# Performance work log

Hardware: AMD Instinct MI355X
Metric: run time of the kernel (lower is better)

The kernel has to match this reference:

```python
import jax, jax.numpy as jnp
import numpy as np

B, L, E, V, H, M, O = 16, 64, 256, 16000, 8, 4, 2
DH = E // H
START = 0

def _pe():
    pos = np.arange(L, dtype=np.float32)[:, None]
    div = np.exp(np.arange(0, E, 2, dtype=np.float32) * (-np.log(10000.0) / E))
    pe = np.zeros((L, E), dtype=np.float32)
    pe[:, 0::2] = np.sin(pos * div)
    pe[:, 1::2] = np.cos(pos * div)
    return jnp.asarray(pe)

PE = _pe()  # [L, E] sinusoidal positional encoding (dropout p=0.0)


def setup_inputs() -> dict:
    key = jax.random.key(0)
    ks = jax.random.split(key, 16)
    g = lambda k, sh, sc: jax.random.normal(k, sh, jnp.float32) * sc
    return {
        'noise': jax.random.normal(ks[0], (B, L), jnp.float32),
        'inEmb_W': g(ks[1], (M, L, L), 1.0 / np.sqrt(L)),   # M stacked Linear(L, L), [in,out] layout
        'inEmb_b': jnp.zeros((M, L), jnp.float32),
        'Wq': g(ks[2], (O, E, E), 1.0 / np.sqrt(E)),
        'bq': jnp.zeros((O, E), jnp.float32),
        'Wk': g(ks[3], (O, E, E), 1.0 / np.sqrt(E)),
        'bk': jnp.zeros((O, E), jnp.float32),
        'Wv': g(ks[4], (O, E, E), 1.0 / np.sqrt(E)),
        'bv': jnp.zeros((O, E), jnp.float32),
        'Wo': g(ks[5], (O, E, E), 1.0 / np.sqrt(E)),
        'bo': jnp.zeros((O, E), jnp.float32),
        'ln_g': jnp.ones((O, E), jnp.float32),
        'ln_b': jnp.zeros((O, E), jnp.float32),
        'emb': g(ks[6], (V, E), 1.0),                       # Word2Vec embedding table
        'soft_W': g(ks[7], (E, V), 1.0 / np.sqrt(E)),       # soft head Linear(E, V)
        'soft_b': jnp.zeros((V,), jnp.float32),
    }


def _ln(x, g, b):
    mu = x.mean(-1, keepdims=True)
    var = ((x - mu) ** 2).mean(-1, keepdims=True)
    return (x - mu) / jnp.sqrt(var + 1e-5) * g + b


def _mha_norm(kv, q, Wq, bq, Wk, bk, Wv, bv, Wo, bo, g, b, kmask):
    # MHAwithNorm: attn(query=q, key=kv, value=kv) -> out proj -> residual -> LayerNorm
    Q = (q @ Wq + bq).reshape(B, L, H, DH)
    K = (kv @ Wk + bk).reshape(B, L, H, DH)
    Vh = (kv @ Wv + bv).reshape(B, L, H, DH)
    s = jnp.einsum('bqhd,bkhd->bhqk', Q, K) / np.sqrt(DH)
    s = jnp.where(kmask[None, None, None, :], s, -1e9)  # only the tok generated positions are valid keys
    a = jax.nn.softmax(s, axis=-1)
    o = jnp.einsum('bhqk,bkhd->bqhd', a, Vh).reshape(B, L, E)
    return _ln(o @ Wo + bo + q, g, b)


def _decode(noise, inEmb_W, inEmb_b, Wq, bq, Wk, bk, Wv, bv, Wo, bo, ln_g, ln_b, emb, soft_W, soft_b):
    w = noise
    for i in range(M):
        w = w @ inEmb_W[i] + inEmb_b[i]
    w = jnp.broadcast_to(w[:, :, None], (B, L, E))  # unsqueeze(-1).repeat(1,1,E)

    Y0 = jnp.zeros((B, L, E), jnp.float32).at[:, 0].set(emb[START] + PE[0])

    def step(Y, tok):
        kmask = jnp.arange(L) < tok  # current sequence length == tok
        out = Y
        for i in range(O):  # cross-attn blocks against w[:, :tok]
            out = _mha_norm(w, out, Wq[i], bq[i], Wk[i], bk[i], Wv[i], bv[i], Wo[i], bo[i], ln_g[i], ln_b[i], kmask)
        for i in range(O):  # same blocks reused as self-attn (faithful to source)
            out = _mha_norm(out, out, Wq[i], bq[i], Wk[i], bk[i], Wv[i], bv[i], Wo[i], bo[i], ln_g[i], ln_b[i], kmask)
        logits = out[:, tok - 1] @ soft_W + soft_b
        probs = jax.nn.softmax(logits, axis=-1)
        nxt = jnp.argmax(probs, axis=-1)  # [B]
        Y = Y.at[:, tok].set(emb[nxt] + PE[tok])
        return Y, (nxt, probs)

    _, (toks, probs) = jax.lax.scan(step, Y0, jnp.arange(1, L))
    return toks, probs  # toks [L-1, B] int, probs [L-1, B, V]


def reference(noise, inEmb_W, inEmb_b, Wq, bq, Wk, bk, Wv, bv, Wo, bo, ln_g, ln_b, emb, soft_W, soft_b):
    toks, _ = _decode(noise, inEmb_W, inEmb_b, Wq, bq, Wk, bk, Wv, bv, Wo, bo, ln_g, ln_b, emb, soft_W, soft_b)
    # torch.stack(out_sent[0]): generated token ids of batch element 0, incl. <START>
    return jnp.concatenate([jnp.array([START], dtype=toks.dtype), toks[:, 0]])
```

## Files before the change

### kernel.cpp

```cpp
#include <hip/hip_runtime.h>
#include <stdint.h>


#define NWG 128
#define NT 256

__device__ __forceinline__ float ld_c(const float* p){
  return __hip_atomic_load(p, __ATOMIC_RELAXED, __HIP_MEMORY_SCOPE_AGENT);
}
__device__ __forceinline__ void st_c(float* p, float v){
  __hip_atomic_store(p, v, __ATOMIC_RELAXED, __HIP_MEMORY_SCOPE_AGENT);
}
__device__ __forceinline__ int ld_fi(const int* p){
  return __hip_atomic_load(p, __ATOMIC_RELAXED, __HIP_MEMORY_SCOPE_AGENT);
}
__device__ __forceinline__ void st_fi(int* p, int v){
  __hip_atomic_store(p, v, __ATOMIC_RELAXED, __HIP_MEMORY_SCOPE_AGENT);
}

__device__ __forceinline__ float wredsum(float v){
#pragma unroll
  for (int m=32;m;m>>=1) v += __shfl_xor(v,m,64);
  return v;
}
__device__ __forceinline__ float wredmax(float v){
#pragma unroll
  for (int m=32;m;m>>=1) v = fmaxf(v,__shfl_xor(v,m,64));
  return v;
}
__device__ __forceinline__ float g32sum(float v){
#pragma unroll
  for (int m=16;m;m>>=1) v += __shfl_xor(v,m,64);
  return v;
}
__device__ __forceinline__ float g32max(float v){
#pragma unroll
  for (int m=16;m;m>>=1) v = fmaxf(v,__shfl_xor(v,m,64));
  return v;
}
__device__ __forceinline__ unsigned long long shflx64(unsigned long long v,int m){
  unsigned int lo=(unsigned int)(v&0xffffffffull), hi=(unsigned int)(v>>32);
  lo=__shfl_xor(lo,m,64); hi=__shfl_xor(hi,m,64);
  return (((unsigned long long)hi)<<32)|(unsigned long long)lo;
}

__device__ __forceinline__ float pe_val(int l, int e){
  int j = e >> 1;
  float dv = expf((float)(2*j) * (-0.035977892078031970f));
  float arg = (float)l * dv;
  return (e & 1) ? cosf(arg) : sinf(arg);
}

__device__ __forceinline__ void a_chain(const float* xrow, float* rrow,
    float* m8, float* redv,
    const float* KAP, const float* BETA, const float* WVEC,
    const float* CC, const float* UT,
    const float* lng, const float* lnb, int tokm, int t){
  const float ISQ = 0.17677669529663687f;
  for (int blk=0; blk<2; blk++){
    const float* src = blk ? rrow : xrow;
    int hh=t>>5, j=t&31;
    float part=0.f;
    for (int jj=j; jj<256; jj+=32) part += src[jj]*KAP[(blk*8+hh)*256+jj];
    part = g32sum(part);
    float alpha = (part + BETA[blk*8+hh]) * ISQ;
    float s1 = (j<tokm)     ? alpha*WVEC[j]    : -3.4e38f;
    float s2 = (j+32<tokm)  ? alpha*WVEC[j+32] : -3.4e38f;
    float mx = g32max(fmaxf(s1,s2));
    float e1 = expf(s1-mx), e2 = expf(s2-mx);
    float sn = e1*((j<tokm)?WVEC[j]:0.f) + e2*((j+32<tokm)?WVEC[j+32]:0.f);
    float sd = e1+e2;
    sn=g32sum(sn); sd=g32sum(sd);
    if (j==0) m8[hh]=sn/sd;
    __syncthreads();
    float x_ = blk ? rrow[t] : xrow[t];
    float z = CC[blk*256+t] + x_;
#pragma unroll
    for (int h2=0;h2<8;h2++) z += m8[h2]*UT[(blk*8+h2)*256+t];
    float ssum=wredsum(z), ssq=wredsum(z*z);
    int lane=t&63, wid=t>>6;
    if (lane==0){ redv[wid]=ssum; redv[4+wid]=ssq; }
    __syncthreads();
    float ts=redv[0]+redv[1]+redv[2]+redv[3];
    float tq=redv[4]+redv[5]+redv[6]+redv[7];
    float mu=ts*(1.f/256.f);
    float var=tq*(1.f/256.f)-mu*mu;
    float rstd=1.f/sqrtf(var+1e-5f);
    float rv=(z-mu)*rstd*lng[blk*256+t]+lnb[blk*256+t];
    __syncthreads();
    rrow[t]=rv;
    __syncthreads();
  }
}

__device__ __forceinline__ void gbar_f(int* arr, int* rel, int ep){
  __syncthreads();
  if (threadIdx.x==0){
    __builtin_amdgcn_fence(__ATOMIC_RELEASE, "agent");
    __hip_atomic_store(arr + blockIdx.x*16, ep, __ATOMIC_RELAXED, __HIP_MEMORY_SCOPE_AGENT);
  }
  if (blockIdx.x==0){
    if (threadIdx.x < NWG){
      while (__hip_atomic_load(arr + threadIdx.x*16, __ATOMIC_RELAXED, __HIP_MEMORY_SCOPE_AGENT) != ep)
        __builtin_amdgcn_s_sleep(1);
    }
    __syncthreads();
    if (threadIdx.x==0)
      __hip_atomic_store(rel, ep, __ATOMIC_RELAXED, __HIP_MEMORY_SCOPE_AGENT);
  }
  if (threadIdx.x==0){
    while (__hip_atomic_load(rel, __ATOMIC_RELAXED, __HIP_MEMORY_SCOPE_AGENT) != ep)
      __builtin_amdgcn_s_sleep(1);
    __builtin_amdgcn_fence(__ATOMIC_ACQUIRE, "agent");
  }
  __syncthreads();
}

__device__ __forceinline__ void gbar_nf(int* arr, int* rel, int ep){
  __syncthreads();
  if (threadIdx.x==0)
    __hip_atomic_store(arr + blockIdx.x*16, ep, __ATOMIC_RELAXED, __HIP_MEMORY_SCOPE_AGENT);
  if (blockIdx.x==0){
    if (threadIdx.x < NWG){
      while (__hip_atomic_load(arr + threadIdx.x*16, __ATOMIC_RELAXED, __HIP_MEMORY_SCOPE_AGENT) != ep)
        __builtin_amdgcn_s_sleep(1);
    }
    __syncthreads();
    if (threadIdx.x==0)
      __hip_atomic_store(rel, ep, __ATOMIC_RELAXED, __HIP_MEMORY_SCOPE_AGENT);
  }
  if (threadIdx.x==0){
    while (__hip_atomic_load(rel, __ATOMIC_RELAXED, __HIP_MEMORY_SCOPE_AGENT) != ep)
      __builtin_amdgcn_s_sleep(1);
  }
  __syncthreads();
}

extern "C" __global__ __launch_bounds__(256, 2)
void gen18124_kernel(const float* __restrict__ noise,
                     const float* __restrict__ iw, const float* __restrict__ ib,
                     const float* __restrict__ Wq, const float* __restrict__ bq,
                     const float* __restrict__ Wk, const float* __restrict__ bk,
                     const float* __restrict__ Wv, const float* __restrict__ bv,
                     const float* __restrict__ Wo, const float* __restrict__ bo,
                     const float* __restrict__ lng, const float* __restrict__ lnb,
                     const float* __restrict__ emb, const float* __restrict__ sw,
                     const float* __restrict__ sb,
                     int* __restrict__ out, float* __restrict__ ws)
{
  const float ISQ = 0.17677669529663687f;
  __shared__ float sm[5376];
  __shared__ unsigned long long redU[4];
  extern __shared__ float swl[];

  float* WVEC = ws;
  float* SKC  = ws+64;
  float* SVC  = ws+576;
  float* KAP  = ws+1088;
  float* UT   = ws+5184;
  float* CC   = ws+9280;
  float* BETA = ws+9792;
  unsigned long long* SLOTS = (unsigned long long*)(ws+9824);
  int* Z3F = (int*)(ws+9952);
  int* ARR = (int*)(ws+10080);
  int* REL = (int*)(ws+12128);
  float* Yg  = ws+14208;
  float* R1  = ws+30592;
  float* QB  = ws+46976;
  float* KB  = ws+63360;
  float* VB  = ws+79744;
  float* R2  = ws+96128;
  float* Z2P = ws+112512;
  float* Z3P = ws+243584;

  const int g = blockIdx.x, t = threadIdx.x;
  int ep = 0;

  {
    const int base = g*125;
#pragma unroll 8
    for (int i=t; i<256*128; i+=NT){
      int e=i>>7, c=i&127;
      float val = 0.f;
      if (c<125) val = sw[e*16000 + base + c];
      swl[i]=val;
    }
  }

  {
    int c0 = 2*g;
    float a0=Wk[t*256+c0],       a1=Wk[t*256+c0+1];
    float a2=Wk[65536+t*256+c0], a3=Wk[65536+t*256+c0+1];
    float a4=Wv[t*256+c0],       a5=Wv[t*256+c0+1];
    float a6=Wv[65536+t*256+c0], a7=Wv[65536+t*256+c0+1];
    a0=wredsum(a0); a1=wredsum(a1); a2=wredsum(a2); a3=wredsum(a3);
    a4=wredsum(a4); a5=wredsum(a5); a6=wredsum(a6); a7=wredsum(a7);
    int lane=t&63, wid=t>>6;
    if (lane==0){
      sm[wid*8+0]=a0; sm[wid*8+1]=a1; sm[wid*8+2]=a2; sm[wid*8+3]=a3;
      sm[wid*8+4]=a4; sm[wid*8+5]=a5; sm[wid*8+6]=a6; sm[wid*8+7]=a7;
    }
    __syncthreads();
    if (t<8){
      float s=sm[t]+sm[8+t]+sm[16+t]+sm[24+t];
      if (t<4) SKC[(t>>1)*256 + c0 + (t&1)] = s;
      else     SVC[((t-4)>>1)*256 + c0 + ((t-4)&1)] = s;
    }
    __syncthreads();
    if (g==0){
      if (t<64) SLOTS[t]=0ull;
      if (t<8)  Z3F[t*16]=0;
      float* wl = sm+64;
      if (t<64) wl[t] = noise[t];
      __syncthreads();
      for (int i=0;i<4;i++){
        float acc=0.f;
        if (t<64){
          for (int in_=0;in_<64;in_++) acc += wl[in_]*iw[(i*64+in_)*64+t];
          acc += ib[i*64+t];
        }
        __syncthreads();
        if (t<64) wl[t]=acc;
        __syncthreads();
      }
      if (t<64) WVEC[t]=wl[t];
    }
    if (g==1){
      Yg[t] = emb[t] + pe_val(0,t);
      if (t==0) out[0]=0;
    }
  }
  gbar_f(ARR,REL,++ep);

  {
    int c0 = 2*g;
    float p00 = bv[t]    *Wo[t*256+c0],        p01 = bv[t]    *Wo[t*256+c0+1];
    float p10 = bv[256+t]*Wo[65536+t*256+c0],  p11 = bv[256+t]*Wo[65536+t*256+c0+1];
    p00=wredsum(p00); p01=wredsum(p01); p10=wredsum(p10); p11=wredsum(p11);
    int lane=t&63, wid=t>>6;
    if (lane==0){ sm[wid*4+0]=p00; sm[wid*4+1]=p01; sm[wid*4+2]=p10; sm[wid*4+3]=p11; }
    __syncthreads();
    if (t<4){
      float s=sm[t]+sm[4+t]+sm[8+t]+sm[12+t];
      int i=t>>1, cl=t&1;
      CC[i*256+c0+cl] = s + bo[i*256+c0+cl];
    }
    if (t<32){
      int i=t>>4, h2=(t>>1)&7, c=c0+(t&1);
      float s=0.f;
      for (int e2=0;e2<32;e2++) s += SVC[i*256+h2*32+e2]*Wo[i*65536+(h2*32+e2)*256+c];
      UT[(i*8+h2)*256+c]=s;
    }
    if (t>=32 && t<64){
      int u=t-32, i=u>>4, h2=(u>>1)&7, e=c0+(u&1);
      float s=0.f;
      for (int c2=0;c2<32;c2++) s += Wq[i*65536+e*256+h2*32+c2]*SKC[i*256+h2*32+c2];
      KAP[(i*8+h2)*256+e]=s;
    }
    if (g==0 && t>=64 && t<80){
      int u=t-64, i=u>>3, h2=u&7;
      float s=0.f;
      for (int c2=0;c2<32;c2++) s += bq[i*256+h2*32+c2]*SKC[i*256+h2*32+c2];
      BETA[i*8+h2]=s;
    }
  }
  gbar_f(ARR,REL,++ep);

  if (g==0){
    float* axr=sm; float* arr=sm+256; float* am8=sm+512; float* ard=sm+528;
    axr[t]=ld_c(&Yg[t]);
    __syncthreads();
    a_chain(axr,arr,am8,ard, KAP,BETA,WVEC,CC,UT,lng,lnb, 1, t);
    st_c(&R1[t], arr[t]);
  }
  gbar_f(ARR,REL,++ep);

  const int h  = g&7;
  const int rg = g>>3;

  for (int tok=1; tok<64; tok++){
    const int n = tok-1;

    {
      float* rows4 = sm;
#pragma unroll
      for (int jj=0;jj<4;jj++) rows4[jj*256+t] = ld_c(&R1[(rg+16*jj)*256+t]);
      if (tok>1 && rg==(n&15)){
        float* axr=sm+2700; float* arr2=sm+2956; float* am8=sm+3212; float* ard=sm+3224;
        unsigned long long s = __hip_atomic_load(&SLOTS[n], __ATOMIC_RELAXED, __HIP_MEMORY_SCOPE_AGENT);
        int v = (int)(~(unsigned int)(s & 0xffffffffull));
        if (h==0 && t==0) out[n]=v;
        axr[t] = emb[v*256+t] + pe_val(n,t);
        if (h==0) st_c(&Yg[n*256+t], axr[t]);
        __syncthreads();
        a_chain(axr,arr2,am8,ard, KAP,BETA,WVEC,CC,UT,lng,lnb, tok, t);
        rows4[(n>>4)*256+t] = arr2[t];
        if (h==0) st_c(&R1[n*256+t], arr2[t]);
      }
      __syncthreads();
      int c=t&31, epp=t>>5;
      const int col=h*32+c;
      float aq[4]={0,0,0,0}, ak[4]={0,0,0,0}, av[4]={0,0,0,0};
#pragma unroll 8
      for (int e=epp*32; e<epp*32+32; e++){
        float wq_=Wq[e*256+col], wk_=Wk[e*256+col], wv_=Wv[e*256+col];
#pragma unroll
        for (int jj=0;jj<4;jj++){ float r=rows4[jj*256+e]; aq[jj]+=r*wq_; ak[jj]+=r*wk_; av[jj]+=r*wv_; }
      }
#pragma unroll
      for (int jj=0;jj<4;jj++){
        aq[jj]+=__shfl_xor(aq[jj],32,64);
        ak[jj]+=__shfl_xor(ak[jj],32,64);
        av[jj]+=__shfl_xor(av[jj],32,64);
      }
      float4* redq=(float4*)(sm+1056); float4* redk=(float4*)(sm+1568); float4* redv4=(float4*)(sm+2080);
      int lane=t&63, wid=t>>6;
      if (lane<32){
        redq[wid*32+lane]=make_float4(aq[0],aq[1],aq[2],aq[3]);
        redk[wid*32+lane]=make_float4(ak[0],ak[1],ak[2],ak[3]);
        redv4[wid*32+lane]=make_float4(av[0],av[1],av[2],av[3]);
      }
      __syncthreads();
      if (t<32){
        float4 A=redq[t],B4=redq[32+t],C4=redq[64+t],D4=redq[96+t];
        float sq[4]={A.x+B4.x+C4.x+D4.x, A.y+B4.y+C4.y+D4.y, A.z+B4.z+C4.z+D4.z, A.w+B4.w+C4.w+D4.w};
        A=redk[t];B4=redk[32+t];C4=redk[64+t];D4=redk[96+t];
        float sk[4]={A.x+B4.x+C4.x+D4.x, A.y+B4.y+C4.y+D4.y, A.z+B4.z+C4.z+D4.z, A.w+B4.w+C4.w+D4.w};
        A=redv4[t];B4=redv4[32+t];C4=redv4[64+t];D4=redv4[96+t];
        float sv[4]={A.x+B4.x+C4.x+D4.x, A.y+B4.y+C4.y+D4.y, A.z+B4.z+C4.z+D4.z, A.w+B4.w+C4.w+D4.w};
        int cc=h*32+t;
        float bq_=bq[cc], bk_=bk[cc], bv_=bv[cc];
#pragma unroll
        for (int jj=0;jj<4;jj++){
          int q_=rg+16*jj;
          if (q_<tok){
            st_c(&QB[q_*256+cc], sq[jj]+bq_);
            st_c(&KB[q_*256+cc], sk[jj]+bk_);
            st_c(&VB[q_*256+cc], sv[jj]+bv_);
          }
        }
      }
    }
    gbar_nf(ARR,REL,++ep);

    {
      float* Ks=sm; float* Vs=sm+2112; float* qrow=sm+4224; float* arow=sm+4352; float* o2s=sm+4608;
      int k=t>>2, f0=(t&3)*8;
      if (k<tok){
#pragma unroll
        for (int i2=0;i2<8;i2++){
          Ks[k*33+f0+i2]=ld_c(&KB[k*256+h*32+f0+i2]);
          Vs[k*33+f0+i2]=ld_c(&VB[k*256+h*32+f0+i2]);
        }
      }
      if (t<128){ int jj=t>>5, c=t&31; int q_=rg+16*jj; if (q_<tok) qrow[jj*32+c]=ld_c(&QB[q_*256+h*32+c]); }
      __syncthreads();
      int w=t>>6, lane=t&63; int q_=rg+16*w; bool ok=q_<tok;
      float sc=-3.4e38f;
      if (ok && lane<tok){
        sc=0.f;
#pragma unroll
        for (int c2=0;c2<32;c2++) sc+=qrow[w*32+c2]*Ks[lane*33+c2];
        sc*=ISQ;
      }
      float mx=wredmax(sc);
      float ex=(ok&&lane<tok)? expf(sc-mx):0.f;
      float sd=wredsum(ex);
      arow[w*64+lane]= ok ? ex/sd : 0.f;
      __syncthreads();
      int j=lane&31, half=lane>>5;
      float oa=0.f;
      if (ok){ for (int k2=half;k2<tok;k2+=2) oa+=arow[w*64+k2]*Vs[k2*33+j]; }
      oa += __shfl_xor(oa,32,64);
      if (lane<32) o2s[w*32+j]=oa;
      __syncthreads();
      float acc[4]={0,0,0,0};
#pragma unroll 8
      for (int j2=0;j2<32;j2++){
        float wv_=Wo[(h*32+j2)*256+t];
#pragma unroll
        for (int jj=0;jj<4;jj++) acc[jj]+=o2s[jj*32+j2]*wv_;
      }
#pragma unroll
      for (int jj=0;jj<4;jj++){ int q2=rg+16*jj; if (q2<tok) st_c(&Z2P[(h*64+q2)*256+t], acc[jj]); }
    }
    gbar_nf(ARR,REL,++ep);

    {
      float* rows4=sm; float* mus=sm+1024;
#pragma unroll
      for (int jj=0;jj<4;jj++){
        int q_=rg+16*jj;
        float z = bo[t] + ld_c(&R1[q_*256+t]);
#pragma unroll
        for (int h2=0;h2<8;h2++) z += ld_c(&Z2P[(h2*64+q_)*256+t]);
        rows4[jj*256+t]=z;
      }
      __syncthreads();
      {
        int w=t>>6, lane=t&63;
        float v0=rows4[w*256+lane], v1=rows4[w*256+64+lane], v2=rows4[w*256+128+lane], v3=rows4[w*256+192+lane];
        float s=v0+v1+v2+v3, sq2=v0*v0+v1*v1+v2*v2+v3*v3;
        s=wredsum(s); sq2=wredsum(sq2);
        if (lane==0){
          float mu=s*(1.f/256.f);
          float var=sq2*(1.f/256.f)-mu*mu;
          mus[w*2]=mu; mus[w*2+1]=1.f/sqrtf(var+1e-5f);
        }
      }
      __syncthreads();
#pragma unroll
      for (int jj=0;jj<4;jj++){
        float mu=mus[jj*2], rstd=mus[jj*2+1];
        float val=(rows4[jj*256+t]-mu)*rstd*lng[t]+lnb[t];
        rows4[jj*256+t]=val;
        int q_=rg+16*jj;
        if (h==0 && q_==n) st_c(&R2[q_*256+t], val);
      }
      __syncthreads();
      int c=t&31, epp=t>>5;
      const int col=h*32+c;
      float aq[4]={0,0,0,0}, ak[4]={0,0,0,0}, av[4]={0,0,0,0};
#pragma unroll 8
      for (int e=epp*32; e<epp*32+32; e++){
        float wq_=Wq[65536+e*256+col], wk_=Wk[65536+e*256+col], wv_=Wv[65536+e*256+col];
#pragma unroll
        for (int jj=0;jj<4;jj++){ float r=rows4[jj*256+e]; aq[jj]+=r*wq_; ak[jj]+=r*wk_; av[jj]+=r*wv_; }
      }
#pragma unroll
      for (int jj=0;jj<4;jj++){
        aq[jj]+=__shfl_xor(aq[jj],32,64);
        ak[jj]+=__shfl_xor(ak[jj],32,64);
        av[jj]+=__shfl_xor(av[jj],32,64);
      }
      float4* redq=(float4*)(sm+1056); float4* redk=(float4*)(sm+1568); float4* redv4=(float4*)(sm+2080);
      int lane=t&63, wid=t>>6;
      if (lane<32){
        redq[wid*32+lane]=make_float4(aq[0],aq[1],aq[2],aq[3]);
        redk[wid*32+lane]=make_float4(ak[0],ak[1],ak[2],ak[3]);
        redv4[wid*32+lane]=make_float4(av[0],av[1],av[2],av[3]);
      }
      __syncthreads();
      if (t<32){
        float4 A=redq[t],B4=redq[32+t],C4=redq[64+t],D4=redq[96+t];
        float sq[4]={A.x+B4.x+C4.x+D4.x, A.y+B4.y+C4.y+D4.y, A.z+B4.z+C4.z+D4.z, A.w+B4.w+C4.w+D4.w};
        A=redk[t];B4=redk[32+t];C4=redk[64+t];D4=redk[96+t];
        float sk[4]={A.x+B4.x+C4.x+D4.x, A.y+B4.y+C4.y+D4.y, A.z+B4.z+C4.z+D4.z, A.w+B4.w+C4.w+D4.w};
        A=redv4[t];B4=redv4[32+t];C4=redv4[64+t];D4=redv4[96+t];
        float sv[4]={A.x+B4.x+C4.x+D4.x, A.y+B4.y+C4.y+D4.y, A.z+B4.z+C4.z+D4.z, A.w+B4.w+C4.w+D4.w};
        int cc=h*32+t;
#pragma unroll
        for (int jj=0;jj<4;jj++){
          int q_=rg+16*jj;
          if (q_<tok){
            st_c(&KB[q_*256+cc], sk[jj]+bk[256+cc]);
            st_c(&VB[q_*256+cc], sv[jj]+bv[256+cc]);
            if (q_==n) st_c(&QB[q_*256+cc], sq[jj]+bq[256+cc]);
          }
        }
      }
    }
    gbar_nf(ARR,REL,++ep);

    {
      float resid = ld_c(&R2[n*256+t]);
      if (g < 8){
        const int hh = g;
        float* Ks=sm; float* Vs=sm+2112; float* qn=sm+4224; float* arow=sm+4352; float* o3s=sm+4608;
        int k=t>>2, f0=(t&3)*8;
        if (k<tok){
#pragma unroll
          for (int i2=0;i2<8;i2++){
            Ks[k*33+f0+i2]=ld_c(&KB[k*256+hh*32+f0+i2]);
            Vs[k*33+f0+i2]=ld_c(&VB[k*256+hh*32+f0+i2]);
          }
        }
        if (t<32) qn[t]=ld_c(&QB[n*256+hh*32+t]);
        __syncthreads();
        int lane=t&63, w=t>>6;
        if (w==0){
          float sc=-3.4e38f;
          if (lane<tok){
            sc=0.f;
#pragma unroll
            for (int c2=0;c2<32;c2++) sc+=qn[c2]*Ks[lane*33+c2];
            sc*=ISQ;
          }
          float mx=wredmax(sc);
          float ex=(lane<tok)? expf(sc-mx):0.f;
          float sd=wredsum(ex);
          arow[lane]=ex/sd;
        }
        __syncthreads();
        if (w==0){
          int j=lane&31, half=lane>>5;
          float oa=0.f;
          for (int k2=half;k2<tok;k2+=2) oa+=arow[k2]*Vs[k2*33+j];
          oa+=__shfl_xor(oa,32,64);
          if (lane<32) o3s[j]=oa;
        }
        __syncthreads();
        float acc=0.f;
#pragma unroll 8
        for (int j2=0;j2<32;j2++) acc+=o3s[j2]*Wo[65536+(hh*32+j2)*256+t];
        st_c(&Z3P[hh*256+t], acc);
        __syncthreads();
        if (t==0) st_fi(Z3F + hh*16, tok);
      } else if (g>=64 && g<127){
        const int q = g-64;
        if (q < tok && tok < 63){
          float* axr=sm; float* arr2=sm+256; float* am8=sm+512; float* ard=sm+528;
          axr[t]=ld_c(&Yg[q*256+t]);
          __syncthreads();
          a_chain(axr,arr2,am8,ard, KAP,BETA,WVEC,CC,UT,lng,lnb, tok+1, t);
          st_c(&R1[q*256+t], arr2[t]);
        }
      }
      if (t<8){ while (ld_fi(Z3F + t*16) < tok) __builtin_amdgcn_s_sleep(1); }
      __syncthreads();
      float* outn=sm; float* redv=sm+256; float* pp=sm+512;
      float z = bo[256+t] + resid;
#pragma unroll
      for (int h2=0;h2<8;h2++) z += ld_c(&Z3P[h2*256+t]);
      float s=wredsum(z), sq2=wredsum(z*z);
      int lane=t&63, wid=t>>6;
      if (lane==0){ redv[wid]=s; redv[4+wid]=sq2; }
      __syncthreads();
      float ts=redv[0]+redv[1]+redv[2]+redv[3];
      float tq=redv[4]+redv[5]+redv[6]+redv[7];
      float mu=ts*(1.f/256.f);
      float var=tq*(1.f/256.f)-mu*mu;
      float rstd=1.f/sqrtf(var+1e-5f);
      outn[t]=(z-mu)*rstd*lng[256+t]+lnb[256+t];
      __syncthreads();
      const int c = t & 127, half = t >> 7;
      float acc = 0.f;
      if (c < 125){
        const int e0 = half*128;
#pragma unroll 8
        for (int e=e0; e<e0+128; e++) acc += outn[e]*swl[e*128+c];
      }
      if (half==1 && c<125) pp[c]=acc;
      __syncthreads();
      unsigned long long key=0ull;
      if (half==0 && c<125){
        int v=g*125+c;
        float a2 = acc + pp[c] + sb[v];
        unsigned int fb=__float_as_uint(a2);
        fb = (fb&0x80000000u)? ~fb : (fb|0x80000000u);
        key=(((unsigned long long)fb)<<32) | (unsigned long long)(~(unsigned int)v);
      }
#pragma unroll
      for (int m=32;m;m>>=1){
        unsigned long long o=shflx64(key,m);
        key = (o>key)? o : key;
      }
      if (lane==0) redU[wid]=key;
      __syncthreads();
      if (t==0){
        unsigned long long kk=redU[0];
        if (redU[1]>kk) kk=redU[1];
        if (redU[2]>kk) kk=redU[2];
        if (redU[3]>kk) kk=redU[3];
        atomicMax(&SLOTS[tok], kk);
      }
    }
    gbar_nf(ARR,REL,++ep);
  }

  if (g==0 && t==0){
    unsigned long long s=__hip_atomic_load(&SLOTS[63],__ATOMIC_RELAXED,__HIP_MEMORY_SCOPE_AGENT);
    out[63]=(int)(~(unsigned int)(s&0xffffffffull));
  }
}

extern "C" void kernel_launch(void* const* d_in, const int* in_sizes, int n_in,
                              void* d_out, int out_size, void* d_ws, size_t ws_size,
                              hipStream_t stream)
{
  (void)in_sizes; (void)n_in; (void)out_size; (void)ws_size;
  hipLaunchKernelGGL(gen18124_kernel, dim3(NWG), dim3(NT), 131072, stream,
    (const float*)d_in[0],  (const float*)d_in[1],  (const float*)d_in[2],
    (const float*)d_in[3],  (const float*)d_in[4],  (const float*)d_in[5],
    (const float*)d_in[6],  (const float*)d_in[7],  (const float*)d_in[8],
    (const float*)d_in[9],  (const float*)d_in[10], (const float*)d_in[11],
    (const float*)d_in[12], (const float*)d_in[13], (const float*)d_in[14],
    (const float*)d_in[15], (int*)d_out, (float*)d_ws);
}
```

Baseline: 4.042 ms.

## Fuse argmax reduction into grid barrier with per-block key slots

Instead of each workgroup doing an atomicMax into a global slot and then passing a generic grid barrier, each block writes its local max key to its own slot and signals arrival. Block 0 waits for all arrivals, reduces the 128 keys itself, and publishes the winning token together with the epoch in a single release word. Every block reads the winner from that word into shared memory, which removes the global atomic and the later slot reload. This adds a serial reduction on block 0 inside the barrier and relies on the token id fitting in 14 bits.

```diff
diff --git a/kernel.cpp b/kernel.cpp
--- a/kernel.cpp
+++ b/kernel.cpp
@@ -5,6 +5,8 @@
 #define NWG 128
 #define NT 256
 
+typedef unsigned long long ull;
+
 __device__ __forceinline__ float ld_c(const float* p){
   return __hip_atomic_load(p, __ATOMIC_RELAXED, __HIP_MEMORY_SCOPE_AGENT);
 }
@@ -17,6 +19,12 @@
 __device__ __forceinline__ void st_fi(int* p, int v){
   __hip_atomic_store(p, v, __ATOMIC_RELAXED, __HIP_MEMORY_SCOPE_AGENT);
 }
+__device__ __forceinline__ ull ld_u64(const ull* p){
+  return __hip_atomic_load(p, __ATOMIC_RELAXED, __HIP_MEMORY_SCOPE_AGENT);
+}
+__device__ __forceinline__ void st_u64(ull* p, ull v){
+  __hip_atomic_store(p, v, __ATOMIC_RELAXED, __HIP_MEMORY_SCOPE_AGENT);
+}
 
 __device__ __forceinline__ float wredsum(float v){
 #pragma unroll
@@ -38,10 +46,10 @@
   for (int m=16;m;m>>=1) v = fmaxf(v,__shfl_xor(v,m,64));
   return v;
 }
-__device__ __forceinline__ unsigned long long shflx64(unsigned long long v,int m){
+__device__ __forceinline__ ull shflx64(ull v,int m){
   unsigned int lo=(unsigned int)(v&0xffffffffull), hi=(unsigned int)(v>>32);
   lo=__shfl_xor(lo,m,64); hi=__shfl_xor(hi,m,64);
-  return (((unsigned long long)hi)<<32)|(unsigned long long)lo;
+  return (((ull)hi)<<32)|(ull)lo;
 }
 
 __device__ __forceinline__ float pe_val(int l, int e){
@@ -150,7 +158,8 @@
 {
   const float ISQ = 0.17677669529663687f;
   __shared__ float sm[5376];
-  __shared__ unsigned long long redU[4];
+  __shared__ ull redU[4];
+  __shared__ int winS;
   extern __shared__ float swl[];
 
   float* WVEC = ws;
@@ -160,10 +169,11 @@
   float* UT   = ws+5184;
   float* CC   = ws+9280;
   float* BETA = ws+9792;
-  unsigned long long* SLOTS = (unsigned long long*)(ws+9824);
   int* Z3F = (int*)(ws+9952);
   int* ARR = (int*)(ws+10080);
   int* REL = (int*)(ws+12128);
+  int* REL2= (int*)(ws+12144);
+  ull* KEY = (ull*)(ws+12160);
   float* Yg  = ws+14208;
   float* R1  = ws+30592;
   float* QB  = ws+46976;
@@ -208,8 +218,8 @@
     }
     __syncthreads();
     if (g==0){
-      if (t<64) SLOTS[t]=0ull;
       if (t<8)  Z3F[t*16]=0;
+      if (t==0) *REL2 = 0;
       float* wl = sm+64;
       if (t<64) wl[t] = noise[t];
       __syncthreads();
@@ -287,8 +297,7 @@
       for (int jj=0;jj<4;jj++) rows4[jj*256+t] = ld_c(&R1[(rg+16*jj)*256+t]);
       if (tok>1 && rg==(n&15)){
         float* axr=sm+2700; float* arr2=sm+2956; float* am8=sm+3212; float* ard=sm+3224;
-        unsigned long long s = __hip_atomic_load(&SLOTS[n], __ATOMIC_RELAXED, __HIP_MEMORY_SCOPE_AGENT);
-        int v = (int)(~(unsigned int)(s & 0xffffffffull));
+        int v = winS;
         if (h==0 && t==0) out[n]=v;
         axr[t] = emb[v*256+t] + pe_val(n,t);
         if (h==0) st_c(&Yg[n*256+t], axr[t]);
@@ -542,36 +551,65 @@
       }
       if (half==1 && c<125) pp[c]=acc;
       __syncthreads();
-      unsigned long long key=0ull;
+      ull key=0ull;
       if (half==0 && c<125){
         int v=g*125+c;
         float a2 = acc + pp[c] + sb[v];
         unsigned int fb=__float_as_uint(a2);
         fb = (fb&0x80000000u)? ~fb : (fb|0x80000000u);
-        key=(((unsigned long long)fb)<<32) | (unsigned long long)(~(unsigned int)v);
+        key=(((ull)fb)<<32) | (ull)(~(unsigned int)v);
       }
 #pragma unroll
       for (int m=32;m;m>>=1){
-        unsigned long long o=shflx64(key,m);
+        ull o=shflx64(key,m);
         key = (o>key)? o : key;
       }
       if (lane==0) redU[wid]=key;
       __syncthreads();
       if (t==0){
-        unsigned long long kk=redU[0];
+        ull kk=redU[0];
         if (redU[1]>kk) kk=redU[1];
         if (redU[2]>kk) kk=redU[2];
         if (redU[3]>kk) kk=redU[3];
-        atomicMax(&SLOTS[tok], kk);
-      }
-    }
-    gbar_nf(ARR,REL,++ep);
-  }
-
-  if (g==0 && t==0){
-    unsigned long long s=__hip_atomic_load(&SLOTS[63],__ATOMIC_RELAXED,__HIP_MEMORY_SCOPE_AGENT);
-    out[63]=(int)(~(unsigned int)(s&0xffffffffull));
-  }
+        st_u64(KEY + g*8, kk);
+      }
+    }
+    {
+      ++ep;
+      __syncthreads();
+      if (t==0)
+        st_fi(ARR + g*16, ep);
+      if (g==0){
+        if (t < NWG){
+          while (ld_fi(ARR + t*16) != ep) __builtin_amdgcn_s_sleep(1);
+        }
+        __syncthreads();
+        ull k = 0ull;
+        if (t < NWG) k = ld_u64(KEY + t*8);
+#pragma unroll
+        for (int m=32;m;m>>=1){
+          ull o=shflx64(k,m);
+          k = (o>k)? o : k;
+        }
+        if ((t&63)==0) redU[t>>6]=k;
+        __syncthreads();
+        if (t==0){
+          ull kk=redU[0];
+          if (redU[1]>kk) kk=redU[1];
+          int v = (int)(~(unsigned int)(kk & 0xffffffffull));
+          st_fi(REL2, (ep<<14) | v);
+        }
+      }
+      if (t==0){
+        int r;
+        while (((r = ld_fi(REL2)) >> 14) != ep) __builtin_amdgcn_s_sleep(1);
+        winS = r & 0x3fff;
+      }
+      __syncthreads();
+    }
+  }
+
+  if (g==0 && t==0) out[63] = winS;
 }
 
 extern "C" void kernel_launch(void* const* d_in, const int* in_sizes, int n_in,
```

New measurement: 4.075 ms. About the same (+0.8%).
